# Kernel tuning notes

Measured on AMD Instinct MI355X. Metric: run time of the kernel, lower is better.

## Reference

```python
import jax, jax.numpy as jnp
import numpy as np

N_NODES = 20000
N_EDGES = 320000
IN_F = 16
OUT_F = 16
EDGE_DIM = 16
EDGE_HID = 64
BN_EPS = 1e-5


def setup_inputs() -> dict:
    key = jax.random.key(0)
    ks = jax.random.split(key, 12)
    inp = {
        "h_neigh": jax.random.normal(ks[0], (N_NODES, IN_F), dtype=jnp.float32),
        "h_self": jax.random.normal(ks[1], (N_NODES, IN_F), dtype=jnp.float32),
        "edge_features": jax.random.normal(ks[2], (N_EDGES, EDGE_DIM), dtype=jnp.float32),
        "src": jax.random.randint(ks[3], (N_EDGES,), 0, N_NODES),
        "dst": jax.random.randint(ks[4], (N_EDGES,), 0, N_NODES),
        # params (xavier-ish scale)
        "W_self": jax.random.normal(ks[5], (IN_F, OUT_F), dtype=jnp.float32) * (2.0 / (IN_F + OUT_F)) ** 0.5,
        "bn_gamma": jnp.ones((OUT_F,), dtype=jnp.float32),
        "bn_beta": jnp.zeros((OUT_F,), dtype=jnp.float32),
        "We1": jax.random.normal(ks[6], (EDGE_DIM, EDGE_HID), dtype=jnp.float32) * (2.0 / (EDGE_DIM + EDGE_HID)) ** 0.5,
        "be1": jnp.zeros((EDGE_HID,), dtype=jnp.float32),
        "We2": jax.random.normal(ks[7], (EDGE_HID, IN_F * OUT_F), dtype=jnp.float32) * (2.0 / (EDGE_HID + IN_F * OUT_F)) ** 0.5,
        "be2": jnp.zeros((IN_F * OUT_F,), dtype=jnp.float32),
    }
    return inp


def reference(h_neigh, h_self, edge_features, src, dst,
              W_self, bn_gamma, bn_beta, We1, be1, We2, be2):
    n_nodes = h_self.shape[0]
    in_f, out_f = W_self.shape
    # edge MLP -> per-edge weight matrix [E, in_f, out_f]
    eh = jax.nn.relu(edge_features @ We1 + be1)
    edge_w = (eh @ We2 + be2).reshape(-1, in_f, out_f)
    # gather src features, per-edge matvec, scatter-sum to dst
    # (sum over in_f commutes with the edge sum-reduce, matching
    #  update_all(u_mul_e, sum) followed by .sum(dim=1))
    msg = jnp.einsum('ei,eio->eo', h_neigh[src], edge_w)  # [E, out_f]
    neigh = jax.ops.segment_sum(msg, dst, num_segments=n_nodes)  # [N, out_f]
    # fc_self: Linear(no bias) -> BatchNorm1d (training stats) -> tanh
    y = h_self @ W_self
    mu = y.mean(axis=0)
    var = y.var(axis=0)
    y = (y - mu) / jnp.sqrt(var + BN_EPS) * bn_gamma + bn_beta
    y = jnp.tanh(y)
    z = jax.nn.relu(y + neigh)
    z_norm = jnp.linalg.norm(z, axis=1, keepdims=True)
    z_norm = jnp.where(z_norm == 0, jnp.ones_like(z_norm), z_norm)
    return z / z_norm
```

## Files before the change

kernel.cpp:

```cpp
#include <hip/hip_runtime.h>
#include <hip/hip_bf16.h>
#include <math.h>

#define NN 20000
#define NE 320000
#define BN_EPS 1e-5f
#define CAP 48
#define CNTP 16

#define MSG_BYTES   (NE * 16 * 4)
#define ELIST_OFF   MSG_BYTES
#define ELIST_BYTES (NN * CAP * 4)
#define CNT_OFF     (ELIST_OFF + ELIST_BYTES)
#define CNT_BYTES   (NN * CNTP * 4)
#define BNACC_OFF   (CNT_OFF + CNT_BYTES)
#define EXTRA_OFF   (BNACC_OFF + 128)
#define EXTRA_BYTES (NN * 16 * 4)
#define Y_OFF       (EXTRA_OFF + EXTRA_BYTES)
#define ZERO_OFF    CNT_OFF
#define ZERO_BYTES  (CNT_BYTES + 128 + EXTRA_BYTES)

typedef __bf16 bf16x8 __attribute__((ext_vector_type(8)));
typedef float  f32x4  __attribute__((ext_vector_type(4)));

union BF8 { bf16x8 v; unsigned short us[8]; unsigned int ui[4]; };

__device__ __forceinline__ unsigned short f2bf(float f) {
    unsigned int u = __builtin_bit_cast(unsigned int, f);
    u += 0x7FFFu + ((u >> 16) & 1u);
    return (unsigned short)(u >> 16);
}
__device__ __forceinline__ float bf2f(unsigned short s) {
    unsigned int u = ((unsigned int)s) << 16;
    return __builtin_bit_cast(float, u);
}
__device__ __forceinline__ unsigned int pack2bf(float a, float b) {
    return (unsigned int)f2bf(a) | ((unsigned int)f2bf(b) << 16);
}

__global__ __launch_bounds__(256, 4) void edge_kernel(
    const float* __restrict__ h_neigh, const float* __restrict__ efeat,
    const int* __restrict__ src, const int* __restrict__ dst,
    const float* __restrict__ We1, const float* __restrict__ be1,
    const float* __restrict__ We2, const float* __restrict__ be2,
    float* __restrict__ msgb, int* __restrict__ elist,
    int* __restrict__ cntp, float* __restrict__ extra,
    const float* __restrict__ h_self, const float* __restrict__ Wsf,
    float* __restrict__ y, float* __restrict__ bnacc)
{
    __shared__ __align__(16) unsigned short A3sw[16 * 2 * 64 * 8];
    __shared__ float red[4][32];

    const int t = threadIdx.x;

    {
        const float4* W2v = (const float4*)We2;
#pragma unroll
        for (int it = 0; it < 16; it++) {
            int c4 = t + 256 * it;
            float4 w = W2v[c4];
            int f = c4 * 4;
            int h = f >> 8, c = f & 255;
            int mb = c >> 4, kb = h >> 5, hh = h & 31, co = c & 15;
            int base = ((mb * 2 + kb) * 64 + (hh >> 3) * 16) * 8 + (hh & 7);
            A3sw[base + (co + 0) * 8] = f2bf(w.x);
            A3sw[base + (co + 1) * 8] = f2bf(w.y);
            A3sw[base + (co + 2) * 8] = f2bf(w.z);
            A3sw[base + (co + 3) * 8] = f2bf(w.w);
        }
    }
    __syncthreads();

    const int L = t & 63, wv = t >> 6;
    const int lo16 = L & 15, q = L >> 4;
    const int qc = q & 1;
    const bool qlow = (q < 2);
    const bool qhi1 = ((q >> 1) != 0);

    BF8 w1h[4], w1l[4];
#pragma unroll
    for (int c = 0; c < 4; c++) {
#pragma unroll
        for (int j = 0; j < 8; j++) {
            float w;
            if (q < 2)                 w = We1[(q * 8 + j) * 64 + c * 16 + lo16];
            else if (q == 2 && j == 0) w = be1[c * 16 + lo16];
            else                       w = 0.f;
            unsigned short h = f2bf(w);
            w1h[c].us[j] = h;
            w1l[c].us[j] = f2bf(w - bf2f(h));
        }
    }

    BF8 be2T;
#pragma unroll
    for (int j = 0; j < 8; j++) {
        float bv = be2[(qc * 8 + j) * 16 + lo16];
        be2T.us[j] = qlow ? f2bf(bv) : (unsigned short)0;
    }

    const int addrA = (((q & 1) * 2 + 0) * 16 + lo16) * 4;
    const int addrB = (((q & 1) * 2 + 1) * 16 + lo16) * 4;

    const int NT = NE / 64;
    int bt = blockIdx.x;
    {
        int e = bt * 64 + wv * 16 + lo16;
        int se = src[e];
        int de = dst[e];
        int kv = 0;
        if (q == 0) kv = atomicAdd(&cntp[de * CNTP], 1);

        while (true) {
            int btn = bt + gridDim.x;
            bool hn = btn < NT;
            int en = 0, sen = 0, den = 0, kvn = 0;
            if (hn) {
                en = btn * 64 + wv * 16 + lo16;
                sen = src[en];
                den = dst[en];
                if (q == 0) kvn = atomicAdd(&cntp[den * CNTP], 1);
            }

            float xr[16];
            {
                const float4* xp = (const float4*)(h_neigh + (size_t)se * 16);
#pragma unroll
                for (int k4 = 0; k4 < 4; k4++) {
                    float4 a = xp[k4];
                    xr[k4*4+0] = a.x; xr[k4*4+1] = a.y; xr[k4*4+2] = a.z; xr[k4*4+3] = a.w;
                }
            }

            BF8 a2h, a2l;
            {
                const float4* ep = (const float4*)(efeat + (size_t)e * 16 + qc * 8);
                float4 e0 = ep[0], e1 = ep[1];
                float ev[8] = {e0.x, e0.y, e0.z, e0.w, e1.x, e1.y, e1.z, e1.w};
#pragma unroll
                for (int j = 0; j < 8; j++) {
                    if (qlow) {
                        unsigned short h = f2bf(ev[j]);
                        a2h.us[j] = h;
                        a2l.us[j] = f2bf(ev[j] - bf2f(h));
                    } else {
                        a2h.us[j] = (q == 2 && j == 0) ? (unsigned short)0x3F80 : (unsigned short)0;
                        a2l.us[j] = 0;
                    }
                }
            }

            float vch[4][4];
#pragma unroll
            for (int c = 0; c < 4; c++) {
                f32x4 c2 = {0.f, 0.f, 0.f, 0.f};
                c2 = __builtin_amdgcn_mfma_f32_16x16x32_bf16(w1h[c].v, a2h.v, c2, 0, 0, 0);
                c2 = __builtin_amdgcn_mfma_f32_16x16x32_bf16(w1l[c].v, a2h.v, c2, 0, 0, 0);
                c2 = __builtin_amdgcn_mfma_f32_16x16x32_bf16(w1h[c].v, a2l.v, c2, 0, 0, 0);
#pragma unroll
                for (int r = 0; r < 4; r++) vch[c][r] = fmaxf(c2[r], 0.f);
            }

            unsigned int dwH[4][2], dwL[4][2];
#pragma unroll
            for (int c = 0; c < 4; c++) {
#pragma unroll
                for (int d = 0; d < 2; d++) {
                    float va = vch[c][2*d], vb = vch[c][2*d+1];
                    unsigned short ha = f2bf(va), hb = f2bf(vb);
                    dwH[c][d] = (unsigned int)ha | ((unsigned int)hb << 16);
                    dwL[c][d] = pack2bf(va - bf2f(ha), vb - bf2f(hb));
                }
            }

            BF8 b3h[2], b3l[2];
#pragma unroll
            for (int kb = 0; kb < 2; kb++) {
#pragma unroll
                for (int tt = 0; tt < 4; tt++) {
                    int d = tt & 1;
                    int addr = (tt >> 1) ? addrB : addrA;
                    int h0 = __builtin_amdgcn_ds_bpermute(addr, (int)dwH[kb*2+0][d]);
                    int h1 = __builtin_amdgcn_ds_bpermute(addr, (int)dwH[kb*2+1][d]);
                    int l0 = __builtin_amdgcn_ds_bpermute(addr, (int)dwL[kb*2+0][d]);
                    int l1 = __builtin_amdgcn_ds_bpermute(addr, (int)dwL[kb*2+1][d]);
                    b3h[kb].ui[tt] = (unsigned int)(qhi1 ? h1 : h0);
                    b3l[kb].ui[tt] = (unsigned int)(qhi1 ? l1 : l0);
                }
            }

            BF8 xT;
#pragma unroll
            for (int j = 0; j < 8; j++)
                xT.us[j] = qlow ? f2bf(xr[qc * 8 + j]) : (unsigned short)0;
            f32x4 msg = {0.f, 0.f, 0.f, 0.f};
            msg = __builtin_amdgcn_mfma_f32_16x16x32_bf16(be2T.v, xT.v, msg, 0, 0, 0);

#pragma unroll 4
            for (int mb = 0; mb < 16; mb++) {
                bf16x8 a3a = *(const bf16x8*)&A3sw[((mb * 2 + 0) * 64 + L) * 8];
                bf16x8 a3b = *(const bf16x8*)&A3sw[((mb * 2 + 1) * 64 + L) * 8];
                f32x4 acc = {0.f, 0.f, 0.f, 0.f};
                acc = __builtin_amdgcn_mfma_f32_16x16x32_bf16(a3a, b3h[0].v, acc, 0, 0, 0);
                acc = __builtin_amdgcn_mfma_f32_16x16x32_bf16(a3b, b3h[1].v, acc, 0, 0, 0);
                acc = __builtin_amdgcn_mfma_f32_16x16x32_bf16(a3a, b3l[0].v, acc, 0, 0, 0);
                acc = __builtin_amdgcn_mfma_f32_16x16x32_bf16(a3b, b3l[1].v, acc, 0, 0, 0);
                float xm = xr[mb];
                msg[0] += xm * acc[0];
                msg[1] += xm * acc[1];
                msg[2] += xm * acc[2];
                msg[3] += xm * acc[3];
            }

            *(float4*)(msgb + (size_t)e * 16 + q * 4) =
                make_float4(msg[0], msg[1], msg[2], msg[3]);

            int kk = __shfl(kv, lo16);
            if (kk < CAP) {
                if (q == 0) elist[de * CAP + kv] = e;
            } else {
                float* xp = extra + (size_t)de * 16 + q * 4;
#pragma unroll
                for (int r = 0; r < 4; r++) atomicAdd(xp + r, msg[r]);
            }

            if (!hn) break;
            bt = btn; e = en; se = sen; de = den; kv = kvn;
        }
    }

    int sb = (int)blockIdx.x - 945;
    if (sb >= 0 && sb < 79) {
        int n = sb * 256 + t;
        bool act = (n < NN);
        float hv[16], yv[16];
        if (act) {
            const float4* h4 = (const float4*)(h_self + (size_t)n * 16);
#pragma unroll
            for (int k = 0; k < 4; k++) {
                float4 a = h4[k];
                hv[4*k+0] = a.x; hv[4*k+1] = a.y; hv[4*k+2] = a.z; hv[4*k+3] = a.w;
            }
        } else {
#pragma unroll
            for (int i = 0; i < 16; i++) hv[i] = 0.f;
        }
#pragma unroll
        for (int o = 0; o < 16; o++) {
            float a = 0.f;
#pragma unroll
            for (int i = 0; i < 16; i++) a += hv[i] * Wsf[i*16 + o];
            yv[o] = a;
        }
        if (act) {
            float4* y4 = (float4*)(y + (size_t)n * 16);
#pragma unroll
            for (int k = 0; k < 4; k++)
                y4[k] = make_float4(yv[4*k+0], yv[4*k+1], yv[4*k+2], yv[4*k+3]);
        }
        int lane = t & 63;
#pragma unroll
        for (int o = 0; o < 16; o++) {
            float a = act ? yv[o] : 0.f;
            float b = act ? yv[o]*yv[o] : 0.f;
#pragma unroll
            for (int off = 32; off > 0; off >>= 1) {
                a += __shfl_down(a, off);
                b += __shfl_down(b, off);
            }
            if (lane == 0) { red[wv][o] = a; red[wv][16 + o] = b; }
        }
        __syncthreads();
        if (t < 32) {
            float s = red[0][t] + red[1][t] + red[2][t] + red[3][t];
            atomicAdd(&bnacc[t], s);
        }
    }
}

__global__ __launch_bounds__(256) void final_kernel(
    const float* __restrict__ msgb, const int* __restrict__ elist,
    const int* __restrict__ cntp, const float* __restrict__ extra,
    const float* __restrict__ y, const float* __restrict__ bnacc,
    const float* __restrict__ gamma, const float* __restrict__ beta,
    float* __restrict__ out)
{
    int tb = blockIdx.x * 256 + threadIdx.x;
    int n = tb >> 2, c = tb & 3;
    if (n >= NN) return;

    int deg = cntp[n * CNTP];
    int m = deg < CAP ? deg : CAP;
    const float4* m4 = (const float4*)msgb;
    const int* el = elist + n * CAP;

    float ax = 0.f, ay = 0.f, az = 0.f, aw = 0.f;
    int k = 0;
    for (; k + 4 <= m; k += 4) {
        int e0 = el[k], e1 = el[k+1], e2 = el[k+2], e3 = el[k+3];
        float4 a0 = m4[(size_t)e0*4 + c];
        float4 a1 = m4[(size_t)e1*4 + c];
        float4 a2 = m4[(size_t)e2*4 + c];
        float4 a3 = m4[(size_t)e3*4 + c];
        ax += (a0.x + a1.x) + (a2.x + a3.x);
        ay += (a0.y + a1.y) + (a2.y + a3.y);
        az += (a0.z + a1.z) + (a2.z + a3.z);
        aw += (a0.w + a1.w) + (a2.w + a3.w);
    }
    for (; k < m; k++) {
        int e0 = el[k];
        float4 a0 = m4[(size_t)e0*4 + c];
        ax += a0.x; ay += a0.y; az += a0.z; aw += a0.w;
    }
    if (deg > CAP) {
        float4 a0 = *(const float4*)(extra + (size_t)n * 16 + c * 4);
        ax += a0.x; ay += a0.y; az += a0.z; aw += a0.w;
    }

    float4 yv4 = ((const float4*)y)[(size_t)n * 4 + c];
    float yv[4] = {yv4.x, yv4.y, yv4.z, yv4.w};
    float nb[4] = {ax, ay, az, aw};

    const float inv_n = 1.f / (float)NN;
    float z[4];
    float ss = 0.f;
#pragma unroll
    for (int r = 0; r < 4; r++) {
        int o = c * 4 + r;
        float mu  = bnacc[o] * inv_n;
        float var = bnacc[16 + o] * inv_n - mu * mu;
        float inv = rsqrtf(var + BN_EPS);
        float yy  = (yv[r] - mu) * inv * gamma[o] + beta[o];
        float tt  = tanhf(yy);
        float zz  = fmaxf(tt + nb[r], 0.f);
        z[r] = zz;
        ss += zz * zz;
    }
    ss += __shfl_xor(ss, 1);
    ss += __shfl_xor(ss, 2);
    float nrm = sqrtf(ss);
    if (nrm == 0.f) nrm = 1.f;
    float rr = 1.f / nrm;
    *(float4*)(out + (size_t)n * 16 + c * 4) =
        make_float4(z[0]*rr, z[1]*rr, z[2]*rr, z[3]*rr);
}

extern "C" void kernel_launch(void* const* d_in, const int* in_sizes, int n_in,
                              void* d_out, int out_size, void* d_ws, size_t ws_size,
                              hipStream_t stream) {
    const float* h_neigh = (const float*)d_in[0];
    const float* h_self  = (const float*)d_in[1];
    const float* efeat   = (const float*)d_in[2];
    const int*   src     = (const int*)d_in[3];
    const int*   dst     = (const int*)d_in[4];
    const float* W_self  = (const float*)d_in[5];
    const float* gamma   = (const float*)d_in[6];
    const float* beta    = (const float*)d_in[7];
    const float* We1     = (const float*)d_in[8];
    const float* be1     = (const float*)d_in[9];
    const float* We2     = (const float*)d_in[10];
    const float* be2     = (const float*)d_in[11];
    float* out = (float*)d_out;

    char* ws = (char*)d_ws;
    float* msgb  = (float*)ws;
    int*   elist = (int*)(ws + ELIST_OFF);
    int*   cntp  = (int*)(ws + CNT_OFF);
    float* bnacc = (float*)(ws + BNACC_OFF);
    float* extra = (float*)(ws + EXTRA_OFF);
    float* y     = (float*)(ws + Y_OFF);

    hipMemsetAsync(ws + ZERO_OFF, 0, ZERO_BYTES, stream);

    edge_kernel<<<1024, 256, 0, stream>>>(
        h_neigh, efeat, src, dst, We1, be1, We2, be2,
        msgb, elist, cntp, extra,
        h_self, W_self, y, bnacc);
    final_kernel<<<(NN * 4 + 255) / 256, 256, 0, stream>>>(
        msgb, elist, cntp, extra, y, bnacc, gamma, beta, out);
}
```

Baseline: 155.6 us.

## Build edge lists in a prologue pass and drop overflow atomic buffer

```diff
diff --git a/kernel.cpp b/kernel.cpp
--- a/kernel.cpp
+++ b/kernel.cpp
@@ -14,11 +14,9 @@
 #define CNT_OFF     (ELIST_OFF + ELIST_BYTES)
 #define CNT_BYTES   (NN * CNTP * 4)
 #define BNACC_OFF   (CNT_OFF + CNT_BYTES)
-#define EXTRA_OFF   (BNACC_OFF + 128)
-#define EXTRA_BYTES (NN * 16 * 4)
-#define Y_OFF       (EXTRA_OFF + EXTRA_BYTES)
+#define Y_OFF       (BNACC_OFF + 128)
 #define ZERO_OFF    CNT_OFF
-#define ZERO_BYTES  (CNT_BYTES + 128 + EXTRA_BYTES)
+#define ZERO_BYTES  (CNT_BYTES + 128)
 
 typedef __bf16 bf16x8 __attribute__((ext_vector_type(8)));
 typedef float  f32x4  __attribute__((ext_vector_type(4)));
@@ -44,7 +42,7 @@
     const float* __restrict__ We1, const float* __restrict__ be1,
     const float* __restrict__ We2, const float* __restrict__ be2,
     float* __restrict__ msgb, int* __restrict__ elist,
-    int* __restrict__ cntp, float* __restrict__ extra,
+    int* __restrict__ cntp,
     const float* __restrict__ h_self, const float* __restrict__ Wsf,
     float* __restrict__ y, float* __restrict__ bnacc)
 {
@@ -69,6 +67,12 @@
             A3sw[base + (co + 3) * 8] = f2bf(w.w);
         }
     }
+
+    for (int i = (int)blockIdx.x * 256 + t; i < NE; i += (int)gridDim.x * 256) {
+        int d0 = dst[i];
+        int k0 = atomicAdd(&cntp[d0 * CNTP], 1);
+        if (k0 < CAP) elist[d0 * CAP + k0] = i;
+    }
     __syncthreads();
 
     const int L = t & 63, wv = t >> 6;
@@ -107,19 +111,14 @@
     {
         int e = bt * 64 + wv * 16 + lo16;
         int se = src[e];
-        int de = dst[e];
-        int kv = 0;
-        if (q == 0) kv = atomicAdd(&cntp[de * CNTP], 1);
 
         while (true) {
             int btn = bt + gridDim.x;
             bool hn = btn < NT;
-            int en = 0, sen = 0, den = 0, kvn = 0;
+            int en = 0, sen = 0;
             if (hn) {
                 en = btn * 64 + wv * 16 + lo16;
                 sen = src[en];
-                den = dst[en];
-                if (q == 0) kvn = atomicAdd(&cntp[den * CNTP], 1);
             }
 
             float xr[16];
@@ -215,17 +214,8 @@
             *(float4*)(msgb + (size_t)e * 16 + q * 4) =
                 make_float4(msg[0], msg[1], msg[2], msg[3]);
 
-            int kk = __shfl(kv, lo16);
-            if (kk < CAP) {
-                if (q == 0) elist[de * CAP + kv] = e;
-            } else {
-                float* xp = extra + (size_t)de * 16 + q * 4;
-#pragma unroll
-                for (int r = 0; r < 4; r++) atomicAdd(xp + r, msg[r]);
-            }
-
             if (!hn) break;
-            bt = btn; e = en; se = sen; de = den; kv = kvn;
+            bt = btn; e = en; se = sen;
         }
     }
 
@@ -280,7 +270,7 @@
 
 __global__ __launch_bounds__(256) void final_kernel(
     const float* __restrict__ msgb, const int* __restrict__ elist,
-    const int* __restrict__ cntp, const float* __restrict__ extra,
+    const int* __restrict__ cntp, const int* __restrict__ dst,
     const float* __restrict__ y, const float* __restrict__ bnacc,
     const float* __restrict__ gamma, const float* __restrict__ beta,
     float* __restrict__ out)
@@ -290,31 +280,35 @@
     if (n >= NN) return;
 
     int deg = cntp[n * CNTP];
-    int m = deg < CAP ? deg : CAP;
     const float4* m4 = (const float4*)msgb;
-    const int* el = elist + n * CAP;
 
     float ax = 0.f, ay = 0.f, az = 0.f, aw = 0.f;
-    int k = 0;
-    for (; k + 4 <= m; k += 4) {
-        int e0 = el[k], e1 = el[k+1], e2 = el[k+2], e3 = el[k+3];
-        float4 a0 = m4[(size_t)e0*4 + c];
-        float4 a1 = m4[(size_t)e1*4 + c];
-        float4 a2 = m4[(size_t)e2*4 + c];
-        float4 a3 = m4[(size_t)e3*4 + c];
-        ax += (a0.x + a1.x) + (a2.x + a3.x);
-        ay += (a0.y + a1.y) + (a2.y + a3.y);
-        az += (a0.z + a1.z) + (a2.z + a3.z);
-        aw += (a0.w + a1.w) + (a2.w + a3.w);
-    }
-    for (; k < m; k++) {
-        int e0 = el[k];
-        float4 a0 = m4[(size_t)e0*4 + c];
-        ax += a0.x; ay += a0.y; az += a0.z; aw += a0.w;
-    }
-    if (deg > CAP) {
-        float4 a0 = *(const float4*)(extra + (size_t)n * 16 + c * 4);
-        ax += a0.x; ay += a0.y; az += a0.z; aw += a0.w;
+    if (deg <= CAP) {
+        const int* el = elist + n * CAP;
+        int k = 0;
+        for (; k + 4 <= deg; k += 4) {
+            int e0 = el[k], e1 = el[k+1], e2 = el[k+2], e3 = el[k+3];
+            float4 a0 = m4[(size_t)e0*4 + c];
+            float4 a1 = m4[(size_t)e1*4 + c];
+            float4 a2 = m4[(size_t)e2*4 + c];
+            float4 a3 = m4[(size_t)e3*4 + c];
+            ax += (a0.x + a1.x) + (a2.x + a3.x);
+            ay += (a0.y + a1.y) + (a2.y + a3.y);
+            az += (a0.z + a1.z) + (a2.z + a3.z);
+            aw += (a0.w + a1.w) + (a2.w + a3.w);
+        }
+        for (; k < deg; k++) {
+            int e0 = el[k];
+            float4 a0 = m4[(size_t)e0*4 + c];
+            ax += a0.x; ay += a0.y; az += a0.z; aw += a0.w;
+        }
+    } else {
+        for (int e0 = 0; e0 < NE; e0++) {
+            if (dst[e0] == n) {
+                float4 a0 = m4[(size_t)e0*4 + c];
+                ax += a0.x; ay += a0.y; az += a0.z; aw += a0.w;
+            }
+        }
     }
 
     float4 yv4 = ((const float4*)y)[(size_t)n * 4 + c];
@@ -367,15 +361,14 @@
     int*   elist = (int*)(ws + ELIST_OFF);
     int*   cntp  = (int*)(ws + CNT_OFF);
     float* bnacc = (float*)(ws + BNACC_OFF);
-    float* extra = (float*)(ws + EXTRA_OFF);
     float* y     = (float*)(ws + Y_OFF);
 
     hipMemsetAsync(ws + ZERO_OFF, 0, ZERO_BYTES, stream);
 
     edge_kernel<<<1024, 256, 0, stream>>>(
         h_neigh, efeat, src, dst, We1, be1, We2, be2,
-        msgb, elist, cntp, extra,
+        msgb, elist, cntp,
         h_self, W_self, y, bnacc);
     final_kernel<<<(NN * 4 + 255) / 256, 256, 0, stream>>>(
-        msgb, elist, cntp, extra, y, bnacc, gamma, beta, out);
-}
+        msgb, elist, cntp, dst, y, bnacc, gamma, beta, out);
+}
```

Result: no change. 156.3 us (+0.4%).
